# Optimization experiments

Measured on AMD Instinct MI355X. Metric: run time of the kernel, lower is better.

## Reference

```python
import jax, jax.numpy as jnp
import numpy as np

B, C, D, H, W = 4, 1, 192, 192, 192
SMALL = 4            # int(192 * bias_scale=0.025)
BIAS_STD = 0.7
MAX_SIGMA = 3.0
TRUNCATE = 4.0
K = 2 * int(TRUNCATE * MAX_SIGMA) + 1   # fixed truncated kernel size = 25
N_LABELS = 32
TABLE = 128          # static remap-table size (>= max source label, >= max dest)


def setup_inputs() -> dict:
    key = jax.random.key(0)
    k1, k2, k3, k4, k5 = jax.random.split(key, 5)
    return {
        "x": jax.random.normal(k1, (B, C, D, H, W), jnp.float32),
        "small_bias": jax.random.normal(k2, (B, 1, SMALL, SMALL, SMALL), jnp.float32),
        "sigma01": jax.random.uniform(k3, (B, 3), jnp.float32),
        "labels": jax.random.randint(k4, (B, 1, D, H, W), 0, N_LABELS, jnp.int32),
        "source_values": jnp.arange(N_LABELS, dtype=jnp.int64),
        "dest_values": jax.random.randint(k5, (N_LABELS,), 0, 100, jnp.int64),
    }


def _lin_weights(n_in, n_out):
    """Dense 1D linear-interp matrix [n_out, n_in], align_corners=True."""
    pos = jnp.linspace(0.0, n_in - 1.0, n_out)
    i0 = jnp.clip(jnp.floor(pos).astype(jnp.int32), 0, n_in - 2)
    f = pos - i0.astype(pos.dtype)
    r = jnp.arange(n_out)
    Wm = jnp.zeros((n_out, n_in), jnp.float32)
    Wm = Wm.at[r, i0].add(1.0 - f).at[r, i0 + 1].add(f)
    return Wm


def _bias_field(small_bias):
    # trilinear align_corners upsample [B,1,s,s,s] -> [B,1,D,H,W], separable
    b = small_bias * BIAS_STD
    b = jnp.einsum('bcxyz,dx->bcdyz', b, _lin_weights(SMALL, D))
    b = jnp.einsum('bcdyz,hy->bcdhz', b, _lin_weights(SMALL, H))
    b = jnp.einsum('bcdhz,wz->bcdhw', b, _lin_weights(SMALL, W))
    return b


def _gauss_kernels(sigma):
    """sigma [3] -> normalized kernels [3, K]; identity (delta) where sigma<0.01."""
    ar = jnp.arange(K, dtype=jnp.float32) - K // 2
    s = jnp.maximum(sigma, 1e-3)[:, None]
    g = jnp.exp(-0.5 * (ar[None, :] ** 2) / (s ** 2))
    g = g / g.sum(-1, keepdims=True)
    delta = jnp.zeros((K,), jnp.float32).at[K // 2].set(1.0)
    return jnp.where(sigma[:, None] >= 0.01, g, delta[None, :])


def _blur_axis(x, k, axis):
    # x [C,D,H,W]; depthwise 1D conv along `axis` with replicate (edge) padding
    p = K // 2
    xm = jnp.moveaxis(x, axis, -1)
    shp = xm.shape
    xm = xm.reshape(-1, 1, shp[-1])
    xm = jnp.pad(xm, ((0, 0), (0, 0), (p, p)), mode='edge')
    out = jax.lax.conv_general_dilated(xm, k.reshape(1, 1, K), (1,), 'VALID')
    return jnp.moveaxis(out.reshape(shp), -1, axis)


def _blur_sample(x, kernels):
    # x [C,D,H,W], kernels [3,K]; separable blur over D,H,W
    for i, ax in enumerate((1, 2, 3)):
        x = _blur_axis(x, kernels[i], ax)
    return x


def reference(x, small_bias, sigma01, labels, source_values, dest_values):
    # 1) bias-field corruption: x * exp(upsampled random field)
    img = x * jnp.exp(_bias_field(small_bias))
    # 2) dynamic per-sample Gaussian blur, sigma in [0, MAX_SIGMA]
    kernels = jax.vmap(_gauss_kernels)(sigma01 * MAX_SIGMA)   # [B,3,K]
    img = jax.vmap(_blur_sample)(img, kernels)
    # 3) label remap via lookup table gather
    mapping = jnp.zeros((TABLE,), jnp.int32).at[source_values].set(
        dest_values.astype(jnp.int32))
    labels_out = mapping[labels]
    return img, labels_out
```

## Files before the change

### kernel.cpp

```cpp
#include <hip/hip_runtime.h>
#include <hip/hip_fp16.h>
#include <cstdint>
#include <cstddef>

#define Bc 4
#define Dd 192
#define Hh 192
#define Ww 192
#define KK 25
#define RR 12
#define VOL (Bc*Dd*Hh*Ww)
#define SP 216
#define SPU (SP/2)
#define SH 98

typedef unsigned short u16;
typedef unsigned int   u32;

__global__ void setup_tables_kernel(const float* __restrict__ sigma01,
                                    const int* __restrict__ src,
                                    const int* __restrict__ dst,
                                    float* __restrict__ kern,
                                    u32* __restrict__ kern2,
                                    int* __restrict__ mapping) {
    int t = threadIdx.x;
    if (t < 128) mapping[t] = 0;
    __syncthreads();
    if (t < 32) {
        int s = src[t];
        if (s >= 0 && s < 128) mapping[s] = dst[t];
    }
    if (t < Bc * 3) {
        float sig = sigma01[t] * 3.0f;
        float s = fmaxf(sig, 1e-3f);
        float g[KK];
        float sum = 0.0f;
        #pragma unroll
        for (int i = 0; i < KK; i++) {
            float a = (float)(i - RR);
            float v = expf(-0.5f * a * a / (s * s));
            g[i] = v; sum += v;
        }
        float inv = 1.0f / sum;
        #pragma unroll
        for (int i = 0; i < KK; i++) {
            float v = g[i] * inv;
            if (sig < 0.01f) v = (i == RR) ? 1.0f : 0.0f;
            kern[t * KK + i] = v;
            u16 hb = __builtin_bit_cast(u16, __float2half(v));
            kern2[t * KK + i] = (u32)hb | ((u32)hb << 16);
        }
    }
}

__global__ __launch_bounds__(1024) void pass_wh_remap_kernel(
    const float* __restrict__ x, u16* __restrict__ outB,
    const float* __restrict__ kern, const u32* __restrict__ kern2,
    const float* __restrict__ sb,
    const int4* __restrict__ labels, float4* __restrict__ lab_out,
    const int* __restrict__ mapping) {
    __shared__ u16 P[Hh * SP];
    __shared__ __attribute__((aligned(16))) float ch[Hh][4];
    const int tid = threadIdx.x;
    const int d = blockIdx.x;
    const int b = blockIdx.y;

    if (tid < Hh * 4) {
        int r = tid >> 2, k = tid & 3;
        float pos_d = d * (3.0f / 191.0f);
        int   id0   = min((int)pos_d, 2);
        float fd    = pos_d - (float)id0;
        float pos_h = r * (3.0f / 191.0f);
        float w0h = fmaxf(0.f, 1.f - fabsf(pos_h));
        float w1h = fmaxf(0.f, 1.f - fabsf(pos_h - 1.f));
        float w2h = fmaxf(0.f, 1.f - fabsf(pos_h - 2.f));
        float w3h = fmaxf(0.f, 1.f - fabsf(pos_h - 3.f));
        const float* sbA = sb + b * 64 + id0 * 16;
        float sj0 = (1.f - fd) * sbA[k]      + fd * sbA[16 + k];
        float sj1 = (1.f - fd) * sbA[4 + k]  + fd * sbA[20 + k];
        float sj2 = (1.f - fd) * sbA[8 + k]  + fd * sbA[24 + k];
        float sj3 = (1.f - fd) * sbA[12 + k] + fd * sbA[28 + k];
        ch[r][k] = (w0h * sj0 + w1h * sj1 + w2h * sj2 + w3h * sj3) * 0.7f;
    }
    __syncthreads();

    const size_t xbase = ((size_t)b * Dd + d) * (size_t)(Hh * Ww);
    #pragma unroll
    for (int it = 0; it < 9; it++) {
        int i4 = it * 1024 + tid;
        int r = i4 / 48, w4 = i4 % 48;
        int w = 4 * w4;
        float4 v = ((const float4*)(x + xbase))[i4];
        float4 cv = *(const float4*)&ch[r][0];
        float rs[4];
        #pragma unroll
        for (int j = 0; j < 4; j++) {
            float pw = (w + j) * (3.0f / 191.0f);
            float b0 = fmaxf(0.f, 1.f - fabsf(pw));
            float b1 = fmaxf(0.f, 1.f - fabsf(pw - 1.f));
            float b2 = fmaxf(0.f, 1.f - fabsf(pw - 2.f));
            float b3 = fmaxf(0.f, 1.f - fabsf(pw - 3.f));
            float bias = b0 * cv.x + b1 * cv.y + b2 * cv.z + b3 * cv.w;
            float val = (j == 0 ? v.x : j == 1 ? v.y : j == 2 ? v.z : v.w);
            rs[j] = val * __expf(bias);
        }
        u32 p0 = (u32)__builtin_bit_cast(u16, __float2half(rs[0])) |
                 ((u32)__builtin_bit_cast(u16, __float2half(rs[1])) << 16);
        u32 p1 = (u32)__builtin_bit_cast(u16, __float2half(rs[2])) |
                 ((u32)__builtin_bit_cast(u16, __float2half(rs[3])) << 16);
        u32* dstp = (u32*)&P[r * SP + RR + w];
        dstp[0] = p0; dstp[1] = p1;
        if (w4 == 0) {
            u16 hv = __builtin_bit_cast(u16, __float2half(rs[0]));
            u32 hh = (u32)hv | ((u32)hv << 16);
            u32* hp = (u32*)&P[r * SP];
            #pragma unroll
            for (int m = 0; m < 6; m++) hp[m] = hh;
        } else if (w4 == 47) {
            u16 hv = __builtin_bit_cast(u16, __float2half(rs[3]));
            u32 hh = (u32)hv | ((u32)hv << 16);
            u32* hp = (u32*)&P[r * SP + RR + Ww];
            #pragma unroll
            for (int m = 0; m < 6; m++) hp[m] = hh;
        }
    }
    __syncthreads();

    {
        float kw[KK];
        const float* kp = kern + (b * 3 + 2) * KK;
        #pragma unroll
        for (int t = 0; t < KK; t++) kw[t] = kp[t];
        const int wv = tid >> 6, ln = tid & 63;
        const int r4 = ln >> 5, c = ln & 31;
        #pragma unroll
        for (int it = 0; it < 6; it++) {
            const int row = wv * 12 + it * 2 + r4;
            const u32* rp = (const u32*)&P[row * SP] + 3 * c;
            u32 wraw[15];
            #pragma unroll
            for (int i = 0; i < 15; i++) wraw[i] = rp[i];
            float win[30];
            #pragma unroll
            for (int i = 0; i < 15; i++) {
                float2 f = __half22float2(__builtin_bit_cast(__half2, wraw[i]));
                win[2 * i] = f.x; win[2 * i + 1] = f.y;
            }
            float acc[6];
            #pragma unroll
            for (int j = 0; j < 6; j++) acc[j] = 0.0f;
            #pragma unroll
            for (int t = 0; t < KK; t++) {
                float kv = kw[t];
                #pragma unroll
                for (int j = 0; j < 6; j++) acc[j] += kv * win[j + t];
            }
            u32* wp = (u32*)&P[row * SP + RR + 6 * c];
            #pragma unroll
            for (int m = 0; m < 3; m++) {
                wp[m] = (u32)__builtin_bit_cast(u16, __float2half(acc[2 * m])) |
                        ((u32)__builtin_bit_cast(u16, __float2half(acc[2 * m + 1])) << 16);
            }
        }
    }
    __syncthreads();

    {
        u32 k2[KK];
        const u32* kp = kern2 + (b * 3 + 1) * KK;
        #pragma unroll
        for (int t = 0; t < KK; t++) k2[t] = kp[t];
        u32* outp = (u32*)(outB + xbase);
        #pragma unroll
        for (int it = 0; it < 2; it++) {
            int item = it * 1024 + tid;
            if (item < 1536) {
                int p = item % 96;
                int g = item / 96;
                int hb = g * 12;
                u32 win[36];
                #pragma unroll
                for (int i = 0; i < 36; i++) {
                    int rr = min(max(hb - RR + i, 0), Hh - 1);
                    win[i] = *((const u32*)&P[rr * SP] + 6 + p);
                }
                __half2 acc[12];
                #pragma unroll
                for (int j = 0; j < 12; j++) acc[j] = __float2half2_rn(0.0f);
                #pragma unroll
                for (int t = 0; t < KK; t++) {
                    __half2 kv = __builtin_bit_cast(__half2, k2[t]);
                    #pragma unroll
                    for (int j = 0; j < 12; j++)
                        acc[j] = __hfma2(kv, __builtin_bit_cast(__half2, win[j + t]), acc[j]);
                }
                #pragma unroll
                for (int j = 0; j < 12; j++)
                    outp[(hb + j) * 96 + p] = __builtin_bit_cast(u32, acc[j]);
            }
        }
    }

    {
        const int bid = b * Dd + d;
        int base = bid * 9216 + tid;
        #pragma unroll
        for (int it = 0; it < 9; it++) {
            int i = base + it * 1024;
            int4 l = labels[i];
            float4 o;
            o.x = (float)mapping[min(max(l.x, 0), 127)];
            o.y = (float)mapping[min(max(l.y, 0), 127)];
            o.z = (float)mapping[min(max(l.z, 0), 127)];
            o.w = (float)mapping[min(max(l.w, 0), 127)];
            lab_out[i] = o;
        }
    }
}

__global__ __launch_bounds__(192) void pass_d_kernel(
    const u16* __restrict__ in, float* __restrict__ img,
    const u32* __restrict__ kern2) {
    __shared__ __attribute__((aligned(16))) u16 T[88 * SH];
    const int tid = threadIdx.x;
    const int w0 = blockIdx.x * 96;
    const int d0 = blockIdx.y * 64;
    const int z = blockIdx.z;
    const int h = z % Hh, b = z / Hh;
    u32 k2[KK];
    const u32* kp = kern2 + b * 3 * KK;
    #pragma unroll
    for (int t = 0; t < KK; t++) k2[t] = kp[t];
    #pragma unroll
    for (int k = 0; k < 6; k++) {
        int idx = k * 192 + tid;
        if (idx < 1056) {
            int r = idx / 12, sg = idx % 12;
            int dd = min(max(d0 + r - RR, 0), Dd - 1);
            uint4 v = *(const uint4*)(in + (((size_t)b * Dd + dd) * Hh + h) * (size_t)Ww + w0 + sg * 8);
            u32* p = (u32*)&T[r * SH + sg * 8];
            p[0] = v.x; p[1] = v.y; p[2] = v.z; p[3] = v.w;
        }
    }
    __syncthreads();
    const int p = tid % 48;
    const int g0 = tid / 48;
    #pragma unroll
    for (int cc = 0; cc < 2; cc++) {
        const int g = g0 + cc * 4;
        const int ob = g * 8;
        u32 win[32];
        #pragma unroll
        for (int i = 0; i < 32; i++) win[i] = *(const u32*)&T[(ob + i) * SH + 2 * p];
        __half2 acc[8];
        #pragma unroll
        for (int j = 0; j < 8; j++) acc[j] = __float2half2_rn(0.0f);
        #pragma unroll
        for (int t = 0; t < KK; t++) {
            __half2 kv = __builtin_bit_cast(__half2, k2[t]);
            #pragma unroll
            for (int j = 0; j < 8; j++)
                acc[j] = __hfma2(kv, __builtin_bit_cast(__half2, win[j + t]), acc[j]);
        }
        #pragma unroll
        for (int j = 0; j < 8; j++) {
            float2 f = __half22float2(acc[j]);
            *(float2*)(img + (((size_t)b * Dd + (d0 + ob + j)) * Hh + h) * (size_t)Ww + w0 + 2 * p) = f;
        }
    }
}

extern "C" void kernel_launch(void* const* d_in, const int* in_sizes, int n_in,
                              void* d_out, int out_size, void* d_ws, size_t ws_size,
                              hipStream_t stream) {
    const float* x          = (const float*)d_in[0];
    const float* small_bias = (const float*)d_in[1];
    const float* sigma01    = (const float*)d_in[2];
    const int*   labels     = (const int*)d_in[3];
    const int*   src        = (const int*)d_in[4];
    const int*   dst        = (const int*)d_in[5];

    float* out     = (float*)d_out;
    float* img     = out;
    float* lab_out = out + (size_t)VOL;

    float* kern    = (float*)d_ws;
    u32*   kern2   = (u32*)((float*)d_ws + 384);
    int*   mapping = (int*)((float*)d_ws + 768);
    u16*   Bb      = (u16*)((char*)d_ws + 8192);

    setup_tables_kernel<<<1, 128, 0, stream>>>(sigma01, src, dst, kern, kern2, mapping);

    pass_wh_remap_kernel<<<dim3(Dd, Bc), 1024, 0, stream>>>(
        x, Bb, kern, kern2, small_bias,
        (const int4*)labels, (float4*)lab_out, mapping);
    pass_d_kernel<<<dim3(Ww / 96, Dd / 64, Bc * Hh), 192, 0, stream>>>(Bb, img, kern2);
}
```

Measured before the change: 156.1 us.

## Split W/H blur blocks into two H-halves with halo rows and 512 threads

The fused bias/W-blur/H-blur kernel now processes half of the H extent per block (96 output rows plus 12-row halos, 120 input rows) with 512 threads, launching twice as many blocks. The aim is to shrink shared memory per block and raise occupancy and grid parallelism. In exchange, each block recomputes the bias and W-blur for 24 halo rows, and the bias coefficients are now stored as half precision. A leftover atomicAnd loop over ch is dead code, since the coefficients are rewritten afterwards.

```diff
diff --git a/kernel.cpp b/kernel.cpp
--- a/kernel.cpp
+++ b/kernel.cpp
@@ -13,6 +13,7 @@
 #define SP 216
 #define SPU (SP/2)
 #define SH 98
+#define RIN 120
 
 typedef unsigned short u16;
 typedef unsigned int   u32;
@@ -53,24 +54,26 @@
     }
 }
 
-__global__ __launch_bounds__(1024) void pass_wh_remap_kernel(
+__global__ __launch_bounds__(512) void pass_wh_remap_kernel(
     const float* __restrict__ x, u16* __restrict__ outB,
     const float* __restrict__ kern, const u32* __restrict__ kern2,
     const float* __restrict__ sb,
     const int4* __restrict__ labels, float4* __restrict__ lab_out,
     const int* __restrict__ mapping) {
-    __shared__ u16 P[Hh * SP];
-    __shared__ __attribute__((aligned(16))) float ch[Hh][4];
+    __shared__ u16 P[RIN * SP];
+    __shared__ u32 ch[RIN][2];
     const int tid = threadIdx.x;
-    const int d = blockIdx.x;
-    const int b = blockIdx.y;
-
-    if (tid < Hh * 4) {
+    const int hx = blockIdx.x;
+    const int d  = blockIdx.y;
+    const int b  = blockIdx.z;
+
+    if (tid < RIN * 4) {
         int r = tid >> 2, k = tid & 3;
+        int hrow = min(max(96 * hx - RR + r, 0), Hh - 1);
         float pos_d = d * (3.0f / 191.0f);
         int   id0   = min((int)pos_d, 2);
         float fd    = pos_d - (float)id0;
-        float pos_h = r * (3.0f / 191.0f);
+        float pos_h = hrow * (3.0f / 191.0f);
         float w0h = fmaxf(0.f, 1.f - fabsf(pos_h));
         float w1h = fmaxf(0.f, 1.f - fabsf(pos_h - 1.f));
         float w2h = fmaxf(0.f, 1.f - fabsf(pos_h - 2.f));
@@ -80,48 +83,82 @@
         float sj1 = (1.f - fd) * sbA[4 + k]  + fd * sbA[20 + k];
         float sj2 = (1.f - fd) * sbA[8 + k]  + fd * sbA[24 + k];
         float sj3 = (1.f - fd) * sbA[12 + k] + fd * sbA[28 + k];
-        ch[r][k] = (w0h * sj0 + w1h * sj1 + w2h * sj2 + w3h * sj3) * 0.7f;
-    }
-    __syncthreads();
-
-    const size_t xbase = ((size_t)b * Dd + d) * (size_t)(Hh * Ww);
+        float cv = (w0h * sj0 + w1h * sj1 + w2h * sj2 + w3h * sj3) * 0.7f;
+        u16 hb = __builtin_bit_cast(u16, __float2half(cv));
+        atomicAnd(&ch[r][k >> 1], ~(0xFFFFu << ((k & 1) * 16)));
+        (void)hb;
+    }
+    __syncthreads();
+    if (tid < RIN) {
+        int r = tid;
+        int hrow = min(max(96 * hx - RR + r, 0), Hh - 1);
+        float pos_d = d * (3.0f / 191.0f);
+        int   id0   = min((int)pos_d, 2);
+        float fd    = pos_d - (float)id0;
+        float pos_h = hrow * (3.0f / 191.0f);
+        float w0h = fmaxf(0.f, 1.f - fabsf(pos_h));
+        float w1h = fmaxf(0.f, 1.f - fabsf(pos_h - 1.f));
+        float w2h = fmaxf(0.f, 1.f - fabsf(pos_h - 2.f));
+        float w3h = fmaxf(0.f, 1.f - fabsf(pos_h - 3.f));
+        const float* sbA = sb + b * 64 + id0 * 16;
+        float c[4];
+        #pragma unroll
+        for (int k = 0; k < 4; k++) {
+            float sj0 = (1.f - fd) * sbA[k]      + fd * sbA[16 + k];
+            float sj1 = (1.f - fd) * sbA[4 + k]  + fd * sbA[20 + k];
+            float sj2 = (1.f - fd) * sbA[8 + k]  + fd * sbA[24 + k];
+            float sj3 = (1.f - fd) * sbA[12 + k] + fd * sbA[28 + k];
+            c[k] = (w0h * sj0 + w1h * sj1 + w2h * sj2 + w3h * sj3) * 0.7f;
+        }
+        ch[r][0] = (u32)__builtin_bit_cast(u16, __float2half(c[0])) |
+                   ((u32)__builtin_bit_cast(u16, __float2half(c[1])) << 16);
+        ch[r][1] = (u32)__builtin_bit_cast(u16, __float2half(c[2])) |
+                   ((u32)__builtin_bit_cast(u16, __float2half(c[3])) << 16);
+    }
+    __syncthreads();
+
+    const size_t pbase = ((size_t)b * Dd + d) * (size_t)(Hh * Ww);
     #pragma unroll
-    for (int it = 0; it < 9; it++) {
-        int i4 = it * 1024 + tid;
-        int r = i4 / 48, w4 = i4 % 48;
-        int w = 4 * w4;
-        float4 v = ((const float4*)(x + xbase))[i4];
-        float4 cv = *(const float4*)&ch[r][0];
-        float rs[4];
-        #pragma unroll
-        for (int j = 0; j < 4; j++) {
-            float pw = (w + j) * (3.0f / 191.0f);
-            float b0 = fmaxf(0.f, 1.f - fabsf(pw));
-            float b1 = fmaxf(0.f, 1.f - fabsf(pw - 1.f));
-            float b2 = fmaxf(0.f, 1.f - fabsf(pw - 2.f));
-            float b3 = fmaxf(0.f, 1.f - fabsf(pw - 3.f));
-            float bias = b0 * cv.x + b1 * cv.y + b2 * cv.z + b3 * cv.w;
-            float val = (j == 0 ? v.x : j == 1 ? v.y : j == 2 ? v.z : v.w);
-            rs[j] = val * __expf(bias);
-        }
-        u32 p0 = (u32)__builtin_bit_cast(u16, __float2half(rs[0])) |
-                 ((u32)__builtin_bit_cast(u16, __float2half(rs[1])) << 16);
-        u32 p1 = (u32)__builtin_bit_cast(u16, __float2half(rs[2])) |
-                 ((u32)__builtin_bit_cast(u16, __float2half(rs[3])) << 16);
-        u32* dstp = (u32*)&P[r * SP + RR + w];
-        dstp[0] = p0; dstp[1] = p1;
-        if (w4 == 0) {
-            u16 hv = __builtin_bit_cast(u16, __float2half(rs[0]));
-            u32 hh = (u32)hv | ((u32)hv << 16);
-            u32* hp = (u32*)&P[r * SP];
+    for (int it = 0; it < 12; it++) {
+        int i4 = it * 512 + tid;
+        if (i4 < RIN * 48) {
+            int r = i4 / 48, w4 = i4 % 48;
+            int w = 4 * w4;
+            int hrow = min(max(96 * hx - RR + r, 0), Hh - 1);
+            float4 v = *(const float4*)(x + pbase + (size_t)hrow * Ww + w);
+            float2 cv01 = __half22float2(__builtin_bit_cast(__half2, ch[r][0]));
+            float2 cv23 = __half22float2(__builtin_bit_cast(__half2, ch[r][1]));
+            float rs[4];
             #pragma unroll
-            for (int m = 0; m < 6; m++) hp[m] = hh;
-        } else if (w4 == 47) {
-            u16 hv = __builtin_bit_cast(u16, __float2half(rs[3]));
-            u32 hh = (u32)hv | ((u32)hv << 16);
-            u32* hp = (u32*)&P[r * SP + RR + Ww];
-            #pragma unroll
-            for (int m = 0; m < 6; m++) hp[m] = hh;
+            for (int j = 0; j < 4; j++) {
+                float pw = (w + j) * (3.0f / 191.0f);
+                float b0 = fmaxf(0.f, 1.f - fabsf(pw));
+                float b1 = fmaxf(0.f, 1.f - fabsf(pw - 1.f));
+                float b2 = fmaxf(0.f, 1.f - fabsf(pw - 2.f));
+                float b3 = fmaxf(0.f, 1.f - fabsf(pw - 3.f));
+                float bias = b0 * cv01.x + b1 * cv01.y + b2 * cv23.x + b3 * cv23.y;
+                float val = (j == 0 ? v.x : j == 1 ? v.y : j == 2 ? v.z : v.w);
+                rs[j] = val * __expf(bias);
+            }
+            u32 p0 = (u32)__builtin_bit_cast(u16, __float2half(rs[0])) |
+                     ((u32)__builtin_bit_cast(u16, __float2half(rs[1])) << 16);
+            u32 p1 = (u32)__builtin_bit_cast(u16, __float2half(rs[2])) |
+                     ((u32)__builtin_bit_cast(u16, __float2half(rs[3])) << 16);
+            u32* dstp = (u32*)&P[r * SP + RR + w];
+            dstp[0] = p0; dstp[1] = p1;
+            if (w4 == 0) {
+                u16 hv = __builtin_bit_cast(u16, __float2half(rs[0]));
+                u32 hh = (u32)hv | ((u32)hv << 16);
+                u32* hp = (u32*)&P[r * SP];
+                #pragma unroll
+                for (int m = 0; m < 6; m++) hp[m] = hh;
+            } else if (w4 == 47) {
+                u16 hv = __builtin_bit_cast(u16, __float2half(rs[3]));
+                u32 hh = (u32)hv | ((u32)hv << 16);
+                u32* hp = (u32*)&P[r * SP + RR + Ww];
+                #pragma unroll
+                for (int m = 0; m < 6; m++) hp[m] = hh;
+            }
         }
     }
     __syncthreads();
@@ -134,32 +171,35 @@
         const int wv = tid >> 6, ln = tid & 63;
         const int r4 = ln >> 5, c = ln & 31;
         #pragma unroll
-        for (int it = 0; it < 6; it++) {
-            const int row = wv * 12 + it * 2 + r4;
-            const u32* rp = (const u32*)&P[row * SP] + 3 * c;
-            u32 wraw[15];
-            #pragma unroll
-            for (int i = 0; i < 15; i++) wraw[i] = rp[i];
-            float win[30];
-            #pragma unroll
-            for (int i = 0; i < 15; i++) {
-                float2 f = __half22float2(__builtin_bit_cast(__half2, wraw[i]));
-                win[2 * i] = f.x; win[2 * i + 1] = f.y;
-            }
-            float acc[6];
-            #pragma unroll
-            for (int j = 0; j < 6; j++) acc[j] = 0.0f;
-            #pragma unroll
-            for (int t = 0; t < KK; t++) {
-                float kv = kw[t];
-                #pragma unroll
-                for (int j = 0; j < 6; j++) acc[j] += kv * win[j + t];
-            }
-            u32* wp = (u32*)&P[row * SP + RR + 6 * c];
-            #pragma unroll
-            for (int m = 0; m < 3; m++) {
-                wp[m] = (u32)__builtin_bit_cast(u16, __float2half(acc[2 * m])) |
-                        ((u32)__builtin_bit_cast(u16, __float2half(acc[2 * m + 1])) << 16);
+        for (int it = 0; it < 8; it++) {
+            const int lr = it * 2 + r4;
+            if (lr < 15) {
+                const int row = wv * 15 + lr;
+                const u32* rp = (const u32*)&P[row * SP] + 3 * c;
+                u32 wraw[15];
+                #pragma unroll
+                for (int i = 0; i < 15; i++) wraw[i] = rp[i];
+                float win[30];
+                #pragma unroll
+                for (int i = 0; i < 15; i++) {
+                    float2 f = __half22float2(__builtin_bit_cast(__half2, wraw[i]));
+                    win[2 * i] = f.x; win[2 * i + 1] = f.y;
+                }
+                float acc[6];
+                #pragma unroll
+                for (int j = 0; j < 6; j++) acc[j] = 0.0f;
+                #pragma unroll
+                for (int t = 0; t < KK; t++) {
+                    float kv = kw[t];
+                    #pragma unroll
+                    for (int j = 0; j < 6; j++) acc[j] += kv * win[j + t];
+                }
+                u32* wp = (u32*)&P[row * SP + RR + 6 * c];
+                #pragma unroll
+                for (int m = 0; m < 3; m++) {
+                    wp[m] = (u32)__builtin_bit_cast(u16, __float2half(acc[2 * m])) |
+                            ((u32)__builtin_bit_cast(u16, __float2half(acc[2 * m + 1])) << 16);
+                }
             }
         }
     }
@@ -170,20 +210,17 @@
         const u32* kp = kern2 + (b * 3 + 1) * KK;
         #pragma unroll
         for (int t = 0; t < KK; t++) k2[t] = kp[t];
-        u32* outp = (u32*)(outB + xbase);
+        u32* outp = (u32*)(outB + pbase);
         #pragma unroll
         for (int it = 0; it < 2; it++) {
-            int item = it * 1024 + tid;
-            if (item < 1536) {
-                int p = item % 96;
+            int item = it * 512 + tid;
+            if (item < 768) {
+                int col = item % 96;
                 int g = item / 96;
-                int hb = g * 12;
                 u32 win[36];
                 #pragma unroll
-                for (int i = 0; i < 36; i++) {
-                    int rr = min(max(hb - RR + i, 0), Hh - 1);
-                    win[i] = *((const u32*)&P[rr * SP] + 6 + p);
-                }
+                for (int i = 0; i < 36; i++)
+                    win[i] = *((const u32*)&P[(g * 12 + i) * SP] + 6 + col);
                 __half2 acc[12];
                 #pragma unroll
                 for (int j = 0; j < 12; j++) acc[j] = __float2half2_rn(0.0f);
@@ -196,17 +233,18 @@
                 }
                 #pragma unroll
                 for (int j = 0; j < 12; j++)
-                    outp[(hb + j) * 96 + p] = __builtin_bit_cast(u32, acc[j]);
+                    outp[(96 * hx + g * 12 + j) * 96 + col] =
+                        __builtin_bit_cast(u32, acc[j]);
             }
         }
     }
 
     {
-        const int bid = b * Dd + d;
-        int base = bid * 9216 + tid;
+        const int bid = ((b * Dd) + d) * 2 + hx;
+        int base = bid * 4608 + tid;
         #pragma unroll
         for (int it = 0; it < 9; it++) {
-            int i = base + it * 1024;
+            int i = base + it * 512;
             int4 l = labels[i];
             float4 o;
             o.x = (float)mapping[min(max(l.x, 0), 127)];
@@ -291,7 +329,7 @@
 
     setup_tables_kernel<<<1, 128, 0, stream>>>(sigma01, src, dst, kern, kern2, mapping);
 
-    pass_wh_remap_kernel<<<dim3(Dd, Bc), 1024, 0, stream>>>(
+    pass_wh_remap_kernel<<<dim3(2, Dd, Bc), 512, 0, stream>>>(
         x, Bb, kern, kern2, small_bias,
         (const int4*)labels, (float4*)lab_out, mapping);
     pass_d_kernel<<<dim3(Ww / 96, Dd / 64, Bc * Hh), 192, 0, stream>>>(Bb, img, kern2);
```

Measured after the change: 152.1 us. 2.6% less time.
